# Kernel optimization log

Hardware: AMD Instinct MI355X
Metric: run time of the kernel (lower is better)

## Reference

```python
import jax, jax.numpy as jnp
import numpy as np

B, Hh, Ww, C = 4, 64, 64, 64


def setup_inputs() -> dict:
    key = jax.random.key(0)
    ks = jax.random.split(key, 5)
    scale = 1.0 / np.sqrt(C)
    return {
        "x": jax.random.normal(ks[0], (B, Hh, Ww, C), dtype=jnp.float32),
        "Wq": jax.random.normal(ks[1], (C, C), dtype=jnp.float32) * scale,
        "bq": jnp.zeros((C,), dtype=jnp.float32),
        "Wk": jax.random.normal(ks[2], (C, C), dtype=jnp.float32) * scale,
        "bk": jnp.zeros((C,), dtype=jnp.float32),
        "Wv": jax.random.normal(ks[3], (C, C), dtype=jnp.float32) * scale,
        "bv": jnp.zeros((C,), dtype=jnp.float32),
        "gamma": jax.random.normal(ks[4], (1,), dtype=jnp.float32) * 0.05,
    }


def reference(x, Wq, bq, Wk, bk, Wv, bv, gamma):
    b, h, w, c = x.shape
    n = h * w
    # 1x1 convs == per-pixel dense projections
    q = (jnp.einsum('bhwc,cf->bhwf', x, Wq) + bq).reshape(b, n, c)
    k = (jnp.einsum('bhwc,cf->bhwf', x, Wk) + bk).reshape(b, n, c)
    v = (jnp.einsum('bhwc,cf->bhwf', x, Wv) + bv).reshape(b, n, c)
    # energy[b, i, j] = <q_i, k_j>; no scaling, softmax over last axis (j)
    energy = jnp.einsum('bic,bjc->bij', q, k)
    attn = jax.nn.softmax(energy, axis=-1)
    # original: transpose(matmul(value^T, attention)) -> out[b,n,c] = sum_m attn[b,m,n] * v[b,m,c]
    out = jnp.einsum('bmn,bmc->bnc', attn, v)
    out = out.reshape(b, h, w, c)
    return gamma * out + x
```

## Files before the change

kernel.cpp:

```cpp
#include <hip/hip_runtime.h>
#include <hip/hip_bf16.h>


typedef __attribute__((ext_vector_type(8))) short short8;
typedef __attribute__((ext_vector_type(4))) short short4b;
typedef __attribute__((ext_vector_type(4))) float f32x4;
typedef __attribute__((ext_vector_type(4))) unsigned int u32x4;
typedef __attribute__((ext_vector_type(2))) unsigned int u32x2;

#define DEV static __device__ __forceinline__
#define LOG2E 1.4426950408889634f

DEV unsigned short f2bf(float f) {
    __hip_bfloat16 h = __float2bfloat16(f);
    return __builtin_bit_cast(unsigned short, h);
}
DEV unsigned int pack2(float lo, float hi) {
    return (unsigned int)f2bf(lo) | ((unsigned int)f2bf(hi) << 16);
}
DEV unsigned int pack2t(float lo, float hi) {
    unsigned int ul = __builtin_bit_cast(unsigned int, lo);
    unsigned int uh = __builtin_bit_cast(unsigned int, hi);
    return (uh & 0xffff0000u) | (ul >> 16);
}
DEV f32x4 MFMA32(short8 a, short8 b, f32x4 c) {
    return __builtin_amdgcn_mfma_f32_16x16x32_bf16(a, b, c, 0, 0, 0);
}
DEV f32x4 MFMA16(short4b a, short4b b, f32x4 c) {
#if __has_builtin(__builtin_amdgcn_mfma_f32_16x16x16_bf16)
    return __builtin_amdgcn_mfma_f32_16x16x16_bf16(a, b, c, 0, 0, 0);
#else
    return __builtin_amdgcn_mfma_f32_16x16x16bf16_1k(a, b, c, 0, 0, 0);
#endif
}
DEV float EXP2(float x) {
#if __has_builtin(__builtin_amdgcn_exp2f)
    return __builtin_amdgcn_exp2f(x);
#else
    return exp2f(x);
#endif
}

#define OFF_Q    0u
#define OFF_K    2097152u
#define OFF_VT   4194304u
#define OFF_WT   6291456u
#define OFF_S    6316032u
#define OFF_LR   6381568u

__global__ __launch_bounds__(256) void k0z(const float* __restrict__ Wq,
                                           const float* __restrict__ Wk,
                                           const float* __restrict__ Wv,
                                           unsigned short* __restrict__ wt,
                                           float* __restrict__ sbuf) {
    int e = blockIdx.x * 256 + threadIdx.x;
    sbuf[e] = 0.0f;
    if (e < 3 * 4096) {
        int w3 = e >> 12, rem = e & 4095, f = rem >> 6, c = rem & 63;
        const float* W = (w3 == 0) ? Wq : (w3 == 1) ? Wk : Wv;
        float s = (w3 == 0) ? LOG2E : 1.0f;
        wt[e] = f2bf(W[c * 64 + f] * s);
    }
}

__global__ __launch_bounds__(256) void k1_proj(const float* __restrict__ x,
                                               const unsigned short* __restrict__ wt,
                                               const float* __restrict__ bq,
                                               const float* __restrict__ bk,
                                               const float* __restrict__ bv,
                                               unsigned short* __restrict__ qg,
                                               unsigned short* __restrict__ kg,
                                               unsigned short* __restrict__ vtg) {
    __shared__ __align__(16) char XT[8192];
    __shared__ __align__(16) char WT1[8192];
    __shared__ __align__(16) char VTILE[9216];
    int t = threadIdx.x, blk = blockIdx.x;
    int w3 = blk >> 8, rb = blk & 255;

    {
        int m = t >> 2, q4 = t & 3;
        const f32x4* xs = (const f32x4*)(x + (size_t)(rb * 64 + m) * 64 + q4 * 16);
        f32x4 fa = xs[0], f2 = xs[1], fc = xs[2], fd = xs[3];
        u32x4 u0 = { pack2(fa[0],fa[1]), pack2(fa[2],fa[3]), pack2(f2[0],f2[1]), pack2(f2[2],f2[3]) };
        u32x4 u1 = { pack2(fc[0],fc[1]), pack2(fc[2],fc[3]), pack2(fd[0],fd[1]), pack2(fd[2],fd[3]) };
        int sw = (m & 7) << 4;
        *(u32x4*)(XT + m * 128 + ((q4 * 32) ^ sw)) = u0;
        *(u32x4*)(XT + m * 128 + ((q4 * 32 + 16) ^ sw)) = u1;
    }
    {
        int f = t >> 2, q4 = t & 3;
        const u32x4* s = (const u32x4*)(wt + w3 * 4096 + f * 64 + q4 * 16);
        u32x4 u0 = s[0], u1 = s[1];
        int sw = (f & 7) << 4;
        *(u32x4*)(WT1 + f * 128 + ((q4 * 32) ^ sw)) = u0;
        *(u32x4*)(WT1 + f * 128 + ((q4 * 32 + 16) ^ sw)) = u1;
    }
    __syncthreads();

    int lane = t & 63, wid = t >> 6, g = lane >> 4, ln = lane & 15;
    int arow = wid * 16 + ln;
    short8 a0 = *(const short8*)(XT + arow * 128 + ((16 * g) ^ ((arow & 7) << 4)));
    short8 a1 = *(const short8*)(XT + arow * 128 + ((64 + 16 * g) ^ ((arow & 7) << 4)));
    const float* bias = (w3 == 0) ? bq : (w3 == 1) ? bk : bv;
    float bscale = (w3 == 0) ? LOG2E : 1.0f;

    #pragma unroll
    for (int fb = 0; fb < 4; ++fb) {
        int frow = fb * 16 + ln;
        short8 b0 = *(const short8*)(WT1 + frow * 128 + ((16 * g) ^ ((frow & 7) << 4)));
        short8 b1 = *(const short8*)(WT1 + frow * 128 + ((64 + 16 * g) ^ ((frow & 7) << 4)));
        f32x4 acc = {0.f, 0.f, 0.f, 0.f};
        acc = MFMA32(a0, b0, acc);
        acc = MFMA32(a1, b1, acc);
        float bval = bias[frow] * bscale;
        if (w3 < 2) {
            unsigned short* dst = (w3 == 0) ? qg : kg;
            int gr = rb * 64 + wid * 16 + 4 * g;
            #pragma unroll
            for (int r = 0; r < 4; ++r)
                dst[(size_t)(gr + r) * 64 + frow] = f2bf(acc[r] + bval);
        } else {
            unsigned short* vt = (unsigned short*)VTILE;
            int mloc = wid * 16 + 4 * g;
            #pragma unroll
            for (int r = 0; r < 4; ++r)
                vt[frow * 72 + mloc + r] = f2bf(acc[r] + bval);
        }
    }
    if (w3 == 2) {
        __syncthreads();
        int f = t >> 2, mq = t & 3;
        u32x4 u0 = *(const u32x4*)(VTILE + f * 144 + mq * 32);
        u32x4 u1 = *(const u32x4*)(VTILE + f * 144 + mq * 32 + 16);
        int b = rb >> 6, n0 = (rb & 63) * 64;
        unsigned short* dst = vtg + (size_t)b * 262144 + f * 4096 + n0 + mq * 16;
        *(u32x4*)(dst) = u0;
        *(u32x4*)(dst + 8) = u1;
    }
}

__global__ __launch_bounds__(256, 4) void k2_rowsum(const unsigned short* __restrict__ qg,
                                                    const unsigned short* __restrict__ kg,
                                                    float* __restrict__ sbuf) {
    __shared__ __align__(16) char KD[2][16384];
    int t = threadIdx.x, blk = blockIdx.x;
    int b = blk >> 8, ns = (blk >> 6) & 3, mb = blk & 63;
    int m0 = mb * 64, nbase = ns * 1024;
    int lane = t & 63, wid = t >> 6, g = lane >> 4, ln = lane & 15;

    short8 a[4][2];
    {
        const unsigned short* qr = qg + (size_t)(b * 4096 + m0 + ln) * 64;
        #pragma unroll
        for (int mi = 0; mi < 4; ++mi) {
            a[mi][0] = *(const short8*)(qr + mi * 1024 + 8 * g);
            a[mi][1] = *(const short8*)(qr + mi * 1024 + 32 + 8 * g);
        }
    }
    int kr = t >> 1, kh = t & 1, ksw = (kr & 7) << 4;
    const unsigned short* kbase = kg + (size_t)(b * 4096 + nbase) * 64;
    {
        const u32x4* s = (const u32x4*)(kbase + (size_t)kr * 64 + kh * 32);
        u32x4 u0 = s[0], u1 = s[1], u2 = s[2], u3 = s[3];
        char* d = KD[0] + kr * 128;
        *(u32x4*)(d + ((kh * 64 +  0) ^ ksw)) = u0;
        *(u32x4*)(d + ((kh * 64 + 16) ^ ksw)) = u1;
        *(u32x4*)(d + ((kh * 64 + 32) ^ ksw)) = u2;
        *(u32x4*)(d + ((kh * 64 + 48) ^ ksw)) = u3;
    }
    __syncthreads();

    f32x4 z = {0.f, 0.f, 0.f, 0.f};
    f32x4 acc[4] = {z, z, z, z};
    int buf = 0;
    for (int nc = 0; nc < 8; ++nc) {
        int nn = (nc < 7) ? nc + 1 : nc;
        const u32x4* s = (const u32x4*)(kbase + (size_t)(nn * 128 + kr) * 64 + kh * 32);
        u32x4 p0 = s[0], p1 = s[1], p2 = s[2], p3 = s[3];
        const char* kt = KD[buf];
        #pragma unroll
        for (int j = 0; j < 2; ++j) {
            int brow = (2 * wid + j) * 16 + ln, bsw = (brow & 7) << 4;
            short8 kb0 = *(const short8*)(kt + brow * 128 + ((16 * g) ^ bsw));
            short8 kb1 = *(const short8*)(kt + brow * 128 + ((64 + 16 * g) ^ bsw));
            #pragma unroll
            for (int mi = 0; mi < 4; ++mi) {
                f32x4 e = MFMA32(a[mi][1], kb1, MFMA32(a[mi][0], kb0, z));
                acc[mi][0] += EXP2(e[0]); acc[mi][1] += EXP2(e[1]);
                acc[mi][2] += EXP2(e[2]); acc[mi][3] += EXP2(e[3]);
            }
        }
        char* d = KD[buf ^ 1] + kr * 128;
        *(u32x4*)(d + ((kh * 64 +  0) ^ ksw)) = p0;
        *(u32x4*)(d + ((kh * 64 + 16) ^ ksw)) = p1;
        *(u32x4*)(d + ((kh * 64 + 32) ^ ksw)) = p2;
        *(u32x4*)(d + ((kh * 64 + 48) ^ ksw)) = p3;
        __syncthreads();
        buf ^= 1;
    }
    #pragma unroll
    for (int mi = 0; mi < 4; ++mi) {
        #pragma unroll
        for (int msk = 1; msk < 16; msk <<= 1) {
            acc[mi][0] += __shfl_xor(acc[mi][0], msk);
            acc[mi][1] += __shfl_xor(acc[mi][1], msk);
            acc[mi][2] += __shfl_xor(acc[mi][2], msk);
            acc[mi][3] += __shfl_xor(acc[mi][3], msk);
        }
    }
    if (ln == 0) {
        #pragma unroll
        for (int mi = 0; mi < 4; ++mi) {
            float* base = sbuf + b * 4096 + m0 + mi * 16 + 4 * g;
            unsafeAtomicAdd(base + 0, acc[mi][0]);
            unsafeAtomicAdd(base + 1, acc[mi][1]);
            unsafeAtomicAdd(base + 2, acc[mi][2]);
            unsafeAtomicAdd(base + 3, acc[mi][3]);
        }
    }
}

__global__ __launch_bounds__(256) void r2_init(const float* __restrict__ sbuf,
                                               float* __restrict__ lrbuf,
                                               const float* __restrict__ x,
                                               float* __restrict__ outp) {
    int tid = blockIdx.x * 256 + threadIdx.x;
    if (tid < 16384) lrbuf[tid] = -__log2f(sbuf[tid]);
    f32x4 v = *(const f32x4*)(x + 4 * (size_t)tid);
    *(f32x4*)(outp + 4 * (size_t)tid) = v;
}

__global__ __launch_bounds__(256, 4) void k3_out(const unsigned short* __restrict__ qg,
                                                 const unsigned short* __restrict__ kg,
                                                 const unsigned short* __restrict__ vtg,
                                                 const float* __restrict__ lrbuf,
                                                 const float* __restrict__ gamma,
                                                 float* __restrict__ outp) {
    __shared__ __align__(16) char QD[2][8192];
    __shared__ __align__(16) char VD[2][8192];
    int t = threadIdx.x, blk = blockIdx.x;
    int b = blk >> 8, ms = (blk >> 6) & 3, nb = blk & 63;
    int n0 = nb * 64, mbase = ms * 1024;
    int lane = t & 63, wid = t >> 6, g = lane >> 4, ln = lane & 15;

    const unsigned short* krp = kg + (size_t)(b * 4096 + n0 + wid * 16 + ln) * 64;
    short8 kb0 = *(const short8*)(krp + 8 * g);
    short8 kb1 = *(const short8*)(krp + 32 + 8 * g);

    int row = t >> 2, q4 = t & 3, sw = (row & 7) << 4;
    const unsigned short* qbase = qg + (size_t)(b * 4096 + mbase + row) * 64 + q4 * 16;
    const unsigned short* vbase = vtg + (size_t)b * 262144 + (size_t)row * 4096 + mbase + q4 * 16;
    {
        u32x4 q0 = *(const u32x4*)(qbase);
        u32x4 q1 = *(const u32x4*)(qbase + 8);
        u32x4 v0 = *(const u32x4*)(vbase);
        u32x4 v1 = *(const u32x4*)(vbase + 8);
        *(u32x4*)(QD[0] + row * 128 + ((q4 * 32) ^ sw)) = q0;
        *(u32x4*)(QD[0] + row * 128 + ((q4 * 32 + 16) ^ sw)) = q1;
        *(u32x4*)(VD[0] + row * 128 + ((q4 * 32) ^ sw)) = v0;
        *(u32x4*)(VD[0] + row * 128 + ((q4 * 32 + 16) ^ sw)) = v1;
    }
    const float* lrb = lrbuf + b * 4096 + mbase + 4 * g;
    f32x4 lc0 = *(const f32x4*)(lrb);
    f32x4 lc1 = *(const f32x4*)(lrb + 16);
    f32x4 lc2 = *(const f32x4*)(lrb + 32);
    f32x4 lc3 = *(const f32x4*)(lrb + 48);
    __syncthreads();

    f32x4 z = {0.f, 0.f, 0.f, 0.f};
    f32x4 oacc[4] = {z, z, z, z};
    int buf = 0;
    for (int mc = 0; mc < 16; ++mc) {
        int nx = (mc < 15) ? mc + 1 : mc;
        u32x4 qp0 = *(const u32x4*)(qbase + (size_t)nx * 64 * 64);
        u32x4 qp1 = *(const u32x4*)(qbase + (size_t)nx * 64 * 64 + 8);
        u32x4 vp0 = *(const u32x4*)(vbase + nx * 64);
        u32x4 vp1 = *(const u32x4*)(vbase + nx * 64 + 8);
        f32x4 ln0 = *(const f32x4*)(lrb + nx * 64);
        f32x4 ln1 = *(const f32x4*)(lrb + nx * 64 + 16);
        f32x4 ln2 = *(const f32x4*)(lrb + nx * 64 + 32);
        f32x4 ln3 = *(const f32x4*)(lrb + nx * 64 + 48);

        const char* qt = QD[buf];
        const char* vt = VD[buf];
        #pragma unroll
        for (int s = 0; s < 4; ++s) {
            int qrow = s * 16 + ln, qsw = (qrow & 7) << 4;
            short8 as0 = *(const short8*)(qt + qrow * 128 + ((16 * g) ^ qsw));
            short8 as1 = *(const short8*)(qt + qrow * 128 + ((64 + 16 * g) ^ qsw));
            f32x4 lv = (s == 0) ? lc0 : (s == 1) ? lc1 : (s == 2) ? lc2 : lc3;
            f32x4 e = MFMA32(as1, kb1, MFMA32(as0, kb0, lv));
            float p0 = EXP2(e[0]), p1 = EXP2(e[1]), p2 = EXP2(e[2]), p3 = EXP2(e[3]);
            u32x2 pw = { pack2t(p0, p1), pack2t(p2, p3) };
            short4b pa = __builtin_bit_cast(short4b, pw);
            #pragma unroll
            for (int fb = 0; fb < 4; ++fb) {
                int vrow = fb * 16 + ln;
                short4b vb = *(const short4b*)(vt + vrow * 128 + ((s * 32 + g * 8) ^ ((vrow & 7) << 4)));
                oacc[fb] = MFMA16(pa, vb, oacc[fb]);
            }
        }
        *(u32x4*)(QD[buf ^ 1] + row * 128 + ((q4 * 32) ^ sw)) = qp0;
        *(u32x4*)(QD[buf ^ 1] + row * 128 + ((q4 * 32 + 16) ^ sw)) = qp1;
        *(u32x4*)(VD[buf ^ 1] + row * 128 + ((q4 * 32) ^ sw)) = vp0;
        *(u32x4*)(VD[buf ^ 1] + row * 128 + ((q4 * 32 + 16) ^ sw)) = vp1;
        lc0 = ln0; lc1 = ln1; lc2 = ln2; lc3 = ln3;
        __syncthreads();
        buf ^= 1;
    }

    float gm = gamma[0];
    int nr = b * 4096 + n0 + wid * 16 + 4 * g;
    #pragma unroll
    for (int fb = 0; fb < 4; ++fb) {
        #pragma unroll
        for (int r = 0; r < 4; ++r)
            unsafeAtomicAdd(outp + (size_t)(nr + r) * 64 + fb * 16 + ln, gm * oacc[fb][r]);
    }
}

extern "C" void kernel_launch(void* const* d_in, const int* in_sizes, int n_in,
                              void* d_out, int out_size, void* d_ws, size_t ws_size,
                              hipStream_t stream) {
    const float* x  = (const float*)d_in[0];
    const float* Wq = (const float*)d_in[1];
    const float* bq = (const float*)d_in[2];
    const float* Wk = (const float*)d_in[3];
    const float* bk = (const float*)d_in[4];
    const float* Wv = (const float*)d_in[5];
    const float* bv = (const float*)d_in[6];
    const float* gm = (const float*)d_in[7];
    char* ws = (char*)d_ws;
    float* outp = (float*)d_out;

    unsigned short* qg  = (unsigned short*)(ws + OFF_Q);
    unsigned short* kg  = (unsigned short*)(ws + OFF_K);
    unsigned short* vtg = (unsigned short*)(ws + OFF_VT);
    unsigned short* wt  = (unsigned short*)(ws + OFF_WT);
    float* sbuf         = (float*)(ws + OFF_S);
    float* lrbuf        = (float*)(ws + OFF_LR);

    k0z<<<64, 256, 0, stream>>>(Wq, Wk, Wv, wt, sbuf);
    k1_proj<<<768, 256, 0, stream>>>(x, wt, bq, bk, bv, qg, kg, vtg);
    k2_rowsum<<<1024, 256, 0, stream>>>(qg, kg, sbuf);
    r2_init<<<1024, 256, 0, stream>>>(sbuf, lrbuf, x, outp);
    k3_out<<<1024, 256, 0, stream>>>(qg, kg, vtg, lrbuf, gm, outp);
}
```

Measured before the change: 134.5 us.

## Fold weight prep into projection, stage Q/K stores, reshape k3 warp tiling

Removes the separate weight-transpose/zero kernel by having each projection block read and convert its weight matrix directly, and zero the row-sum buffer there. Q/K outputs are now staged through shared memory and written out as coalesced 16-byte stores. In the output kernel each warp now handles a 2x2 grid of 16-row sub-tiles (two query sub-tiles times two key sub-tiles). This reuses the V fragments and LDS Q reads across two key sub-tiles. The cost is twice the accumulator registers and more redundant weight reads per projection block.

Measured after the change: 149.8 us. 1.11x slower.

```diff
diff --git a/kernel.cpp b/kernel.cpp
--- a/kernel.cpp
+++ b/kernel.cpp
@@ -44,38 +44,27 @@
 #define OFF_Q    0u
 #define OFF_K    2097152u
 #define OFF_VT   4194304u
-#define OFF_WT   6291456u
-#define OFF_S    6316032u
-#define OFF_LR   6381568u
-
-__global__ __launch_bounds__(256) void k0z(const float* __restrict__ Wq,
-                                           const float* __restrict__ Wk,
-                                           const float* __restrict__ Wv,
-                                           unsigned short* __restrict__ wt,
-                                           float* __restrict__ sbuf) {
-    int e = blockIdx.x * 256 + threadIdx.x;
-    sbuf[e] = 0.0f;
-    if (e < 3 * 4096) {
-        int w3 = e >> 12, rem = e & 4095, f = rem >> 6, c = rem & 63;
-        const float* W = (w3 == 0) ? Wq : (w3 == 1) ? Wk : Wv;
-        float s = (w3 == 0) ? LOG2E : 1.0f;
-        wt[e] = f2bf(W[c * 64 + f] * s);
-    }
-}
+#define OFF_S    6291456u
+#define OFF_LR   6356992u
 
 __global__ __launch_bounds__(256) void k1_proj(const float* __restrict__ x,
-                                               const unsigned short* __restrict__ wt,
+                                               const float* __restrict__ Wq,
                                                const float* __restrict__ bq,
+                                               const float* __restrict__ Wk,
                                                const float* __restrict__ bk,
+                                               const float* __restrict__ Wv,
                                                const float* __restrict__ bv,
                                                unsigned short* __restrict__ qg,
                                                unsigned short* __restrict__ kg,
-                                               unsigned short* __restrict__ vtg) {
+                                               unsigned short* __restrict__ vtg,
+                                               float* __restrict__ sbuf) {
     __shared__ __align__(16) char XT[8192];
     __shared__ __align__(16) char WT1[8192];
-    __shared__ __align__(16) char VTILE[9216];
+    __shared__ __align__(16) char OT[9216];
     int t = threadIdx.x, blk = blockIdx.x;
     int w3 = blk >> 8, rb = blk & 255;
+
+    if (w3 == 0 && t < 64) sbuf[rb * 64 + t] = 0.0f;
 
     {
         int m = t >> 2, q4 = t & 3;
@@ -87,10 +76,18 @@
         *(u32x4*)(XT + m * 128 + ((q4 * 32) ^ sw)) = u0;
         *(u32x4*)(XT + m * 128 + ((q4 * 32 + 16) ^ sw)) = u1;
     }
+    const float* W = (w3 == 0) ? Wq : (w3 == 1) ? Wk : Wv;
+    float wscale = (w3 == 0) ? LOG2E : 1.0f;
     {
         int f = t >> 2, q4 = t & 3;
-        const u32x4* s = (const u32x4*)(wt + w3 * 4096 + f * 64 + q4 * 16);
-        u32x4 u0 = s[0], u1 = s[1];
+        unsigned int u[8];
+        #pragma unroll
+        for (int i = 0; i < 8; ++i) {
+            float lo = W[(size_t)(q4 * 16 + 2 * i) * 64 + f] * wscale;
+            float hi = W[(size_t)(q4 * 16 + 2 * i + 1) * 64 + f] * wscale;
+            u[i] = pack2(lo, hi);
+        }
+        u32x4 u0 = { u[0], u[1], u[2], u[3] }, u1 = { u[4], u[5], u[6], u[7] };
         int sw = (f & 7) << 4;
         *(u32x4*)(WT1 + f * 128 + ((q4 * 32) ^ sw)) = u0;
         *(u32x4*)(WT1 + f * 128 + ((q4 * 32 + 16) ^ sw)) = u1;
@@ -102,8 +99,8 @@
     short8 a0 = *(const short8*)(XT + arow * 128 + ((16 * g) ^ ((arow & 7) << 4)));
     short8 a1 = *(const short8*)(XT + arow * 128 + ((64 + 16 * g) ^ ((arow & 7) << 4)));
     const float* bias = (w3 == 0) ? bq : (w3 == 1) ? bk : bv;
-    float bscale = (w3 == 0) ? LOG2E : 1.0f;
-
+
+    unsigned short* ot = (unsigned short*)OT;
     #pragma unroll
     for (int fb = 0; fb < 4; ++fb) {
         int frow = fb * 16 + ln;
@@ -112,30 +109,33 @@
         f32x4 acc = {0.f, 0.f, 0.f, 0.f};
         acc = MFMA32(a0, b0, acc);
         acc = MFMA32(a1, b1, acc);
-        float bval = bias[frow] * bscale;
+        float bval = bias[frow] * wscale;
+        int mloc = wid * 16 + 4 * g;
         if (w3 < 2) {
-            unsigned short* dst = (w3 == 0) ? qg : kg;
-            int gr = rb * 64 + wid * 16 + 4 * g;
             #pragma unroll
             for (int r = 0; r < 4; ++r)
-                dst[(size_t)(gr + r) * 64 + frow] = f2bf(acc[r] + bval);
+                ot[(mloc + r) * 72 + frow] = f2bf(acc[r] + bval);
         } else {
-            unsigned short* vt = (unsigned short*)VTILE;
-            int mloc = wid * 16 + 4 * g;
             #pragma unroll
             for (int r = 0; r < 4; ++r)
-                vt[frow * 72 + mloc + r] = f2bf(acc[r] + bval);
-        }
-    }
-    if (w3 == 2) {
-        __syncthreads();
-        int f = t >> 2, mq = t & 3;
-        u32x4 u0 = *(const u32x4*)(VTILE + f * 144 + mq * 32);
-        u32x4 u1 = *(const u32x4*)(VTILE + f * 144 + mq * 32 + 16);
-        int b = rb >> 6, n0 = (rb & 63) * 64;
-        unsigned short* dst = vtg + (size_t)b * 262144 + f * 4096 + n0 + mq * 16;
-        *(u32x4*)(dst) = u0;
-        *(u32x4*)(dst + 8) = u1;
+                ot[frow * 72 + mloc + r] = f2bf(acc[r] + bval);
+        }
+    }
+    __syncthreads();
+    {
+        int rr = t >> 2, mq = t & 3;
+        u32x4 u0 = *(const u32x4*)(OT + rr * 144 + mq * 32);
+        u32x4 u1 = *(const u32x4*)(OT + rr * 144 + mq * 32 + 16);
+        if (w3 < 2) {
+            unsigned short* dst = ((w3 == 0) ? qg : kg) + (size_t)(rb * 64 + rr) * 64 + mq * 16;
+            *(u32x4*)(dst) = u0;
+            *(u32x4*)(dst + 8) = u1;
+        } else {
+            int b = rb >> 6, n0 = (rb & 63) * 64;
+            unsigned short* dst = vtg + (size_t)b * 262144 + (size_t)rr * 4096 + n0 + mq * 16;
+            *(u32x4*)(dst) = u0;
+            *(u32x4*)(dst + 8) = u1;
+        }
     }
 }
 
@@ -242,10 +242,15 @@
     int b = blk >> 8, ms = (blk >> 6) & 3, nb = blk & 63;
     int n0 = nb * 64, mbase = ms * 1024;
     int lane = t & 63, wid = t >> 6, g = lane >> 4, ln = lane & 15;
-
-    const unsigned short* krp = kg + (size_t)(b * 4096 + n0 + wid * 16 + ln) * 64;
-    short8 kb0 = *(const short8*)(krp + 8 * g);
-    short8 kb1 = *(const short8*)(krp + 32 + 8 * g);
+    int wm = wid >> 1, wn = wid & 1;
+
+    short8 kb[2][2];
+    #pragma unroll
+    for (int jj = 0; jj < 2; ++jj) {
+        const unsigned short* krp = kg + (size_t)(b * 4096 + n0 + (2 * wn + jj) * 16 + ln) * 64;
+        kb[jj][0] = *(const short8*)(krp + 8 * g);
+        kb[jj][1] = *(const short8*)(krp + 32 + 8 * g);
+    }
 
     int row = t >> 2, q4 = t & 3, sw = (row & 7) << 4;
     const unsigned short* qbase = qg + (size_t)(b * 4096 + mbase + row) * 64 + q4 * 16;
@@ -261,14 +266,12 @@
         *(u32x4*)(VD[0] + row * 128 + ((q4 * 32 + 16) ^ sw)) = v1;
     }
     const float* lrb = lrbuf + b * 4096 + mbase + 4 * g;
-    f32x4 lc0 = *(const f32x4*)(lrb);
-    f32x4 lc1 = *(const f32x4*)(lrb + 16);
-    f32x4 lc2 = *(const f32x4*)(lrb + 32);
-    f32x4 lc3 = *(const f32x4*)(lrb + 48);
+    f32x4 lcA = *(const f32x4*)(lrb + (2 * wm) * 16);
+    f32x4 lcB = *(const f32x4*)(lrb + (2 * wm + 1) * 16);
     __syncthreads();
 
     f32x4 z = {0.f, 0.f, 0.f, 0.f};
-    f32x4 oacc[4] = {z, z, z, z};
+    f32x4 oacc[2][4] = { {z, z, z, z}, {z, z, z, z} };
     int buf = 0;
     for (int mc = 0; mc < 16; ++mc) {
         int nx = (mc < 15) ? mc + 1 : mc;
@@ -276,46 +279,57 @@
         u32x4 qp1 = *(const u32x4*)(qbase + (size_t)nx * 64 * 64 + 8);
         u32x4 vp0 = *(const u32x4*)(vbase + nx * 64);
         u32x4 vp1 = *(const u32x4*)(vbase + nx * 64 + 8);
-        f32x4 ln0 = *(const f32x4*)(lrb + nx * 64);
-        f32x4 ln1 = *(const f32x4*)(lrb + nx * 64 + 16);
-        f32x4 ln2 = *(const f32x4*)(lrb + nx * 64 + 32);
-        f32x4 ln3 = *(const f32x4*)(lrb + nx * 64 + 48);
+        f32x4 lnA = *(const f32x4*)(lrb + nx * 64 + (2 * wm) * 16);
+        f32x4 lnB = *(const f32x4*)(lrb + nx * 64 + (2 * wm + 1) * 16);
 
         const char* qt = QD[buf];
         const char* vt = VD[buf];
         #pragma unroll
-        for (int s = 0; s < 4; ++s) {
+        for (int sub = 0; sub < 2; ++sub) {
+            int s = 2 * wm + sub;
             int qrow = s * 16 + ln, qsw = (qrow & 7) << 4;
             short8 as0 = *(const short8*)(qt + qrow * 128 + ((16 * g) ^ qsw));
             short8 as1 = *(const short8*)(qt + qrow * 128 + ((64 + 16 * g) ^ qsw));
-            f32x4 lv = (s == 0) ? lc0 : (s == 1) ? lc1 : (s == 2) ? lc2 : lc3;
-            f32x4 e = MFMA32(as1, kb1, MFMA32(as0, kb0, lv));
-            float p0 = EXP2(e[0]), p1 = EXP2(e[1]), p2 = EXP2(e[2]), p3 = EXP2(e[3]);
-            u32x2 pw = { pack2t(p0, p1), pack2t(p2, p3) };
-            short4b pa = __builtin_bit_cast(short4b, pw);
-            #pragma unroll
-            for (int fb = 0; fb < 4; ++fb) {
-                int vrow = fb * 16 + ln;
-                short4b vb = *(const short4b*)(vt + vrow * 128 + ((s * 32 + g * 8) ^ ((vrow & 7) << 4)));
-                oacc[fb] = MFMA16(pa, vb, oacc[fb]);
+            short4b vb0, vb1, vb2, vb3;
+            {
+                int so = s * 32 + g * 8;
+                vb0 = *(const short4b*)(vt + (0 * 16 + ln) * 128 + (so ^ (((0 * 16 + ln) & 7) << 4)));
+                vb1 = *(const short4b*)(vt + (1 * 16 + ln) * 128 + (so ^ (((1 * 16 + ln) & 7) << 4)));
+                vb2 = *(const short4b*)(vt + (2 * 16 + ln) * 128 + (so ^ (((2 * 16 + ln) & 7) << 4)));
+                vb3 = *(const short4b*)(vt + (3 * 16 + ln) * 128 + (so ^ (((3 * 16 + ln) & 7) << 4)));
+            }
+            f32x4 lv = sub ? lcB : lcA;
+            #pragma unroll
+            for (int jj = 0; jj < 2; ++jj) {
+                f32x4 e = MFMA32(as1, kb[jj][1], MFMA32(as0, kb[jj][0], lv));
+                float p0 = EXP2(e[0]), p1 = EXP2(e[1]), p2 = EXP2(e[2]), p3 = EXP2(e[3]);
+                u32x2 pw = { pack2t(p0, p1), pack2t(p2, p3) };
+                short4b pa = __builtin_bit_cast(short4b, pw);
+                oacc[jj][0] = MFMA16(pa, vb0, oacc[jj][0]);
+                oacc[jj][1] = MFMA16(pa, vb1, oacc[jj][1]);
+                oacc[jj][2] = MFMA16(pa, vb2, oacc[jj][2]);
+                oacc[jj][3] = MFMA16(pa, vb3, oacc[jj][3]);
             }
         }
         *(u32x4*)(QD[buf ^ 1] + row * 128 + ((q4 * 32) ^ sw)) = qp0;
         *(u32x4*)(QD[buf ^ 1] + row * 128 + ((q4 * 32 + 16) ^ sw)) = qp1;
         *(u32x4*)(VD[buf ^ 1] + row * 128 + ((q4 * 32) ^ sw)) = vp0;
         *(u32x4*)(VD[buf ^ 1] + row * 128 + ((q4 * 32 + 16) ^ sw)) = vp1;
-        lc0 = ln0; lc1 = ln1; lc2 = ln2; lc3 = ln3;
+        lcA = lnA; lcB = lnB;
         __syncthreads();
         buf ^= 1;
     }
 
     float gm = gamma[0];
-    int nr = b * 4096 + n0 + wid * 16 + 4 * g;
     #pragma unroll
-    for (int fb = 0; fb < 4; ++fb) {
-        #pragma unroll
-        for (int r = 0; r < 4; ++r)
-            unsafeAtomicAdd(outp + (size_t)(nr + r) * 64 + fb * 16 + ln, gm * oacc[fb][r]);
+    for (int jj = 0; jj < 2; ++jj) {
+        int nr = b * 4096 + n0 + (2 * wn + jj) * 16 + 4 * g;
+        #pragma unroll
+        for (int fb = 0; fb < 4; ++fb) {
+            #pragma unroll
+            for (int r = 0; r < 4; ++r)
+                unsafeAtomicAdd(outp + (size_t)(nr + r) * 64 + fb * 16 + ln, gm * oacc[jj][fb][r]);
+        }
     }
 }
 
@@ -336,12 +350,10 @@
     unsigned short* qg  = (unsigned short*)(ws + OFF_Q);
     unsigned short* kg  = (unsigned short*)(ws + OFF_K);
     unsigned short* vtg = (unsigned short*)(ws + OFF_VT);
-    unsigned short* wt  = (unsigned short*)(ws + OFF_WT);
     float* sbuf         = (float*)(ws + OFF_S);
     float* lrbuf        = (float*)(ws + OFF_LR);
 
-    k0z<<<64, 256, 0, stream>>>(Wq, Wk, Wv, wt, sbuf);
-    k1_proj<<<768, 256, 0, stream>>>(x, wt, bq, bk, bv, qg, kg, vtg);
+    k1_proj<<<768, 256, 0, stream>>>(x, Wq, bq, Wk, bk, Wv, bv, qg, kg, vtg, sbuf);
     k2_rowsum<<<1024, 256, 0, stream>>>(qg, kg, sbuf);
     r2_init<<<1024, 256, 0, stream>>>(sbuf, lrbuf, x, outp);
     k3_out<<<1024, 256, 0, stream>>>(qg, kg, vtg, lrbuf, gm, outp);
```
